# Kernel tuning notes

Measured on AMD Instinct MI355X. Metric: run time of the kernel, lower is better.

The kernel has to match this reference:

```python
import jax, jax.numpy as jnp
import numpy as np

BATCH, OUT, M, IN = 128, 256, 8, 512

def setup_inputs() -> dict:
    key = jax.random.key(0)
    k1, k2 = jax.random.split(key)
    x = jax.random.normal(k1, (BATCH, M, IN), dtype=jnp.float32)
    DNM_W = jax.random.normal(k2, (OUT, M, IN), dtype=jnp.float32)
    return {"x": x, "DNM_W": DNM_W}

def reference(x, DNM_W):
    # broadcast mul: (i,1,j,k) * (1,b,j,k) -> (i,b,j,k)
    z = jax.nn.sigmoid(x[:, None, :, :] * DNM_W[None, :, :, :])
    z = jnp.sum(z, axis=3)   # (i,b,j): sum over input_size
    z = jnp.prod(z, axis=2)  # (i,b):   prod over M branches
    # normalize(rate=1, dim=1): scale rows to sum 1, then standardize (unbiased std)
    total = jnp.sum(z, axis=1, keepdims=True)
    z = z / total
    mean = jnp.mean(z, axis=1, keepdims=True)
    std = jnp.std(z, axis=1, keepdims=True, ddof=1)  # torch.std is unbiased
    return (z - mean) / std
```

## Files before the change

kernel.cpp:

```cpp
#include <hip/hip_runtime.h>
#include <hip/hip_bf16.h>

#define BATCH 128
#define NOUT  256
#define MB    8
#define IN    512

#define THREADS 256
#define TI 32
#define TB 32
#define CH 128
#define CH4 (CH/4)
#define PLANE (BATCH*NOUT)

typedef float v2f __attribute__((ext_vector_type(2)));

__device__ __forceinline__ float fast_exp2(float v) {
#if __has_builtin(__builtin_amdgcn_exp2f)
  return __builtin_amdgcn_exp2f(v);
#else
  return exp2f(v);
#endif
}
__device__ __forceinline__ float fast_rcp(float v) {
#if __has_builtin(__builtin_amdgcn_rcpf)
  return __builtin_amdgcn_rcpf(v);
#else
  return 1.0f / v;
#endif
}

__device__ __forceinline__ float sig4(v2f p02, v2f p13) {
  float e0 = fast_exp2(p02.x), e2 = fast_exp2(p02.y);
  float e1 = fast_exp2(p13.x), e3 = fast_exp2(p13.y);
  v2f f02 = {e0, e2}; f02 += 1.0f;
  v2f f13 = {e1, e3}; f13 += 1.0f;
  v2f prod = f02 * f13;
  v2f sum  = f02 + f13;
  v2f prodsw = __builtin_shufflevector(prod, prod, 1, 0);
  v2f t = sum * prodsw;
  float num = t.x + t.y;
  float den = prod.x * prod.y;
  return num * fast_rcp(den);
}

template<int JPB, int KCB>
__global__ __launch_bounds__(THREADS, 4) void dnm_partial_kernel(
    const float* __restrict__ x, const float* __restrict__ w,
    float* __restrict__ part)
{
  __shared__ float4 xs4[TI * 32];
  __shared__ float4 ws4[TB * 32];

  const int t   = threadIdx.x;
  const int ti2 = t >> 4;
  const int tb2 = t & 15;
  const int b0  = blockIdx.x * TB;
  const int i0  = blockIdx.y * TI;
  constexpr int KG = (IN / CH) / KCB;
  const int j0  = (blockIdx.z / KG) * JPB;
  const int q0  = (blockIdx.z % KG) * KCB;

  const float4* gx = (const float4*)x;
  const float4* gw = (const float4*)w;
  const float NEG_LOG2E = -1.4426950408889634f;

  float p00 = 1.0f, p01 = 1.0f, p10 = 1.0f, p11 = 1.0f;
  #pragma unroll
  for (int jj = 0; jj < JPB; ++jj) {
    const int j = j0 + jj;
    float s00 = 0.0f, s01 = 0.0f, s10 = 0.0f, s11 = 0.0f;
    #pragma unroll
    for (int cc = 0; cc < KCB; ++cc) {
      const int q = q0 + cc;
      __syncthreads();
      #pragma unroll
      for (int p = 0; p < (2 * TI * CH4) / THREADS; ++p) {
        int idx = t + p * THREADS;
        int r = idx >> 5, c4 = idx & 31;
        int c4s = c4 ^ ((r >> 1) & 7);
        if (r < TI) {
          float4 xv = gx[(size_t)((i0 + r) * MB + j) * (IN / 4) + q * CH4 + c4];
          xv.x *= NEG_LOG2E; xv.y *= NEG_LOG2E; xv.z *= NEG_LOG2E; xv.w *= NEG_LOG2E;
          xs4[r * 32 + c4s] = xv;
        } else {
          ws4[(r - TI) * 32 + c4s] =
              gw[(size_t)((b0 + r - TI) * MB + j) * (IN / 4) + q * CH4 + c4];
        }
      }
      __syncthreads();
      const int sx = ti2 & 7, sw = tb2 & 7;
      const float4* __restrict__ xb0 = &xs4[(2 * ti2) * 32];
      const float4* __restrict__ wb0 = &ws4[(2 * tb2) * 32];
      #pragma unroll 4
      for (int k4 = 0; k4 < CH4; ++k4) {
        int kx = k4 ^ sx, kw = k4 ^ sw;
        float4 xv0 = xb0[kx], xv1 = xb0[32 + kx];
        float4 wv0 = wb0[kw], wv1 = wb0[32 + kw];
        v2f x0a = {xv0.x, xv0.z}, x0b = {xv0.y, xv0.w};
        v2f x1a = {xv1.x, xv1.z}, x1b = {xv1.y, xv1.w};
        v2f w0a = {wv0.x, wv0.z}, w0b = {wv0.y, wv0.w};
        v2f w1a = {wv1.x, wv1.z}, w1b = {wv1.y, wv1.w};
        s00 += sig4(x0a * w0a, x0b * w0b);
        s01 += sig4(x0a * w1a, x0b * w1b);
        s10 += sig4(x1a * w0a, x1b * w0b);
        s11 += sig4(x1a * w1a, x1b * w1b);
      }
    }
    p00 *= s00; p01 *= s01; p10 *= s10; p11 *= s11;
  }
  float* dst = part + (size_t)blockIdx.z * PLANE;
  const int i = i0 + 2 * ti2, b = b0 + 2 * tb2;
  dst[(size_t)i * NOUT + b]           = p00;
  dst[(size_t)i * NOUT + b + 1]       = p01;
  dst[(size_t)(i + 1) * NOUT + b]     = p10;
  dst[(size_t)(i + 1) * NOUT + b + 1] = p11;
}

__device__ __forceinline__ float block_sum(float v, float* red) {
  #pragma unroll
  for (int o = 32; o > 0; o >>= 1) v += __shfl_down(v, o, 64);
  int lane = threadIdx.x & 63, wid = threadIdx.x >> 6;
  __syncthreads();
  if (lane == 0) red[wid] = v;
  __syncthreads();
  return red[0] + red[1] + red[2] + red[3];
}

template<int JG, int KG>
__global__ __launch_bounds__(256) void dnm_norm_kernel(
    const float* __restrict__ part, float* __restrict__ out)
{
  __shared__ float red[4];
  const int i = blockIdx.x;
  const int t = threadIdx.x;
  float z = 1.0f;
  #pragma unroll
  for (int j = 0; j < JG; ++j) {
    float s = 0.0f;
    #pragma unroll
    for (int q = 0; q < KG; ++q)
      s += part[(size_t)(j * KG + q) * PLANE + (size_t)i * NOUT + t];
    z *= s;
  }
  float S  = block_sum(z, red);
  float zn = z / S;
  float m  = block_sum(zn, red) * (1.0f / NOUT);
  float dv = zn - m;
  float v  = block_sum(dv * dv, red) * (1.0f / (NOUT - 1));
  out[(size_t)i * NOUT + t] = dv / sqrtf(v);
}

extern "C" void kernel_launch(void* const* d_in, const int* in_sizes, int n_in,
                              void* d_out, int out_size, void* d_ws, size_t ws_size,
                              hipStream_t stream) {
  const float* x = (const float*)d_in[0];
  const float* w = (const float*)d_in[1];
  float* out = (float*)d_out;

  const size_t plane_bytes = (size_t)PLANE * sizeof(float);

  if (ws_size >= 32 * plane_bytes) {
    float* part = (float*)d_ws;
    dim3 gridA(NOUT / TB, BATCH / TI, 32);
    dnm_partial_kernel<1, 1><<<gridA, THREADS, 0, stream>>>(x, w, part);
    dnm_norm_kernel<8, 4><<<dim3(BATCH), 256, 0, stream>>>(part, out);
  } else if (ws_size >= plane_bytes) {
    float* part = (float*)d_ws;
    dim3 gridA(NOUT / TB, BATCH / TI, 1);
    dnm_partial_kernel<8, 4><<<gridA, THREADS, 0, stream>>>(x, w, part);
    dnm_norm_kernel<1, 1><<<dim3(BATCH), 256, 0, stream>>>(part, out);
  } else {
    float* part = out;
    dim3 gridA(NOUT / TB, BATCH / TI, 1);
    dnm_partial_kernel<8, 4><<<gridA, THREADS, 0, stream>>>(x, w, part);
    dnm_norm_kernel<1, 1><<<dim3(BATCH), 256, 0, stream>>>(part, out);
  }
}
```

Measured before the change: 86.70 us.

## Widen register tile to 2x4 outputs per thread with padded x shared layout

Each thread now computes a 2x4 block of (batch, out) sums instead of 2x2, with the out-tile doubled to 64 and the K chunk halved to 64, so the split-K grid grows to 64 planes. The x shared tile uses a padded stride of 17 float4 instead of an XOR swizzle, W keeps a swizzle keyed on groups of four rows, and partial results are written as float4. The aim is fewer shared-memory loads per sigmoid evaluation and wider stores. In exchange the norm kernel must read and sum twice as many partial planes, the workspace needed grows, and register pressure rises.

```diff
diff --git a/kernel.cpp b/kernel.cpp
--- a/kernel.cpp
+++ b/kernel.cpp
@@ -8,9 +8,10 @@
 
 #define THREADS 256
 #define TI 32
-#define TB 32
-#define CH 128
+#define TB 64
+#define CH 64
 #define CH4 (CH/4)
+#define XST 17
 #define PLANE (BATCH*NOUT)
 
 typedef float v2f __attribute__((ext_vector_type(2)));
@@ -39,9 +40,7 @@
   v2f sum  = f02 + f13;
   v2f prodsw = __builtin_shufflevector(prod, prod, 1, 0);
   v2f t = sum * prodsw;
-  float num = t.x + t.y;
-  float den = prod.x * prod.y;
-  return num * fast_rcp(den);
+  return (t.x + t.y) * fast_rcp(prod.x * prod.y);
 }
 
 template<int JPB, int KCB>
@@ -49,72 +48,82 @@
     const float* __restrict__ x, const float* __restrict__ w,
     float* __restrict__ part)
 {
-  __shared__ float4 xs4[TI * 32];
-  __shared__ float4 ws4[TB * 32];
+  __shared__ float4 xs4[TI * XST];
+  __shared__ float4 ws4[TB * CH4];
 
-  const int t   = threadIdx.x;
-  const int ti2 = t >> 4;
-  const int tb2 = t & 15;
-  const int b0  = blockIdx.x * TB;
-  const int i0  = blockIdx.y * TI;
+  const int t  = threadIdx.x;
+  const int ti = t >> 4;
+  const int n  = t & 15;
+  const int b0 = blockIdx.x * TB;
+  const int i0 = blockIdx.y * TI;
   constexpr int KG = (IN / CH) / KCB;
-  const int j0  = (blockIdx.z / KG) * JPB;
-  const int q0  = (blockIdx.z % KG) * KCB;
+  const int j0 = (blockIdx.z / KG) * JPB;
+  const int q0 = (blockIdx.z % KG) * KCB;
 
   const float4* gx = (const float4*)x;
   const float4* gw = (const float4*)w;
   const float NEG_LOG2E = -1.4426950408889634f;
 
-  float p00 = 1.0f, p01 = 1.0f, p10 = 1.0f, p11 = 1.0f;
+  float p00=1.f,p01=1.f,p02_=1.f,p03=1.f, p10=1.f,p11=1.f,p12=1.f,p13_=1.f;
   #pragma unroll
   for (int jj = 0; jj < JPB; ++jj) {
     const int j = j0 + jj;
-    float s00 = 0.0f, s01 = 0.0f, s10 = 0.0f, s11 = 0.0f;
+    float s00=0.f,s01=0.f,s02=0.f,s03=0.f, s10=0.f,s11=0.f,s12=0.f,s13=0.f;
     #pragma unroll
     for (int cc = 0; cc < KCB; ++cc) {
       const int q = q0 + cc;
       __syncthreads();
       #pragma unroll
-      for (int p = 0; p < (2 * TI * CH4) / THREADS; ++p) {
+      for (int p = 0; p < (TI + TB) * CH4 / THREADS; ++p) {
         int idx = t + p * THREADS;
-        int r = idx >> 5, c4 = idx & 31;
-        int c4s = c4 ^ ((r >> 1) & 7);
+        int r = idx >> 4, c4 = idx & 15;
         if (r < TI) {
           float4 xv = gx[(size_t)((i0 + r) * MB + j) * (IN / 4) + q * CH4 + c4];
           xv.x *= NEG_LOG2E; xv.y *= NEG_LOG2E; xv.z *= NEG_LOG2E; xv.w *= NEG_LOG2E;
-          xs4[r * 32 + c4s] = xv;
+          xs4[r * XST + c4] = xv;
         } else {
-          ws4[(r - TI) * 32 + c4s] =
-              gw[(size_t)((b0 + r - TI) * MB + j) * (IN / 4) + q * CH4 + c4];
+          int rw = r - TI;
+          int c4s = c4 ^ ((rw >> 2) & 7);
+          ws4[rw * CH4 + c4s] = gw[(size_t)((b0 + rw) * MB + j) * (IN / 4) + q * CH4 + c4];
         }
       }
       __syncthreads();
-      const int sx = ti2 & 7, sw = tb2 & 7;
-      const float4* __restrict__ xb0 = &xs4[(2 * ti2) * 32];
-      const float4* __restrict__ wb0 = &ws4[(2 * tb2) * 32];
+      const float4* __restrict__ xr0 = &xs4[(2 * ti)     * XST];
+      const float4* __restrict__ xr1 = &xs4[(2 * ti + 1) * XST];
+      const float4* __restrict__ wr  = &ws4[(4 * n) * CH4];
+      const int sw = n & 7;
       #pragma unroll 4
       for (int k4 = 0; k4 < CH4; ++k4) {
-        int kx = k4 ^ sx, kw = k4 ^ sw;
-        float4 xv0 = xb0[kx], xv1 = xb0[32 + kx];
-        float4 wv0 = wb0[kw], wv1 = wb0[32 + kw];
+        float4 xv0 = xr0[k4], xv1 = xr1[k4];
+        int kw = k4 ^ sw;
+        float4 wv0 = wr[0 * CH4 + kw];
+        float4 wv1 = wr[1 * CH4 + kw];
+        float4 wv2 = wr[2 * CH4 + kw];
+        float4 wv3 = wr[3 * CH4 + kw];
         v2f x0a = {xv0.x, xv0.z}, x0b = {xv0.y, xv0.w};
         v2f x1a = {xv1.x, xv1.z}, x1b = {xv1.y, xv1.w};
-        v2f w0a = {wv0.x, wv0.z}, w0b = {wv0.y, wv0.w};
-        v2f w1a = {wv1.x, wv1.z}, w1b = {wv1.y, wv1.w};
-        s00 += sig4(x0a * w0a, x0b * w0b);
-        s01 += sig4(x0a * w1a, x0b * w1b);
-        s10 += sig4(x1a * w0a, x1b * w0b);
-        s11 += sig4(x1a * w1a, x1b * w1b);
+        v2f wa, wb;
+        wa = (v2f){wv0.x, wv0.z}; wb = (v2f){wv0.y, wv0.w};
+        s00 += sig4(x0a * wa, x0b * wb);
+        s10 += sig4(x1a * wa, x1b * wb);
+        wa = (v2f){wv1.x, wv1.z}; wb = (v2f){wv1.y, wv1.w};
+        s01 += sig4(x0a * wa, x0b * wb);
+        s11 += sig4(x1a * wa, x1b * wb);
+        wa = (v2f){wv2.x, wv2.z}; wb = (v2f){wv2.y, wv2.w};
+        s02 += sig4(x0a * wa, x0b * wb);
+        s12 += sig4(x1a * wa, x1b * wb);
+        wa = (v2f){wv3.x, wv3.z}; wb = (v2f){wv3.y, wv3.w};
+        s03 += sig4(x0a * wa, x0b * wb);
+        s13 += sig4(x1a * wa, x1b * wb);
       }
     }
-    p00 *= s00; p01 *= s01; p10 *= s10; p11 *= s11;
+    p00 *= s00; p01 *= s01; p02_ *= s02; p03 *= s03;
+    p10 *= s10; p11 *= s11; p12 *= s12; p13_ *= s13;
   }
-  float* dst = part + (size_t)blockIdx.z * PLANE;
-  const int i = i0 + 2 * ti2, b = b0 + 2 * tb2;
-  dst[(size_t)i * NOUT + b]           = p00;
-  dst[(size_t)i * NOUT + b + 1]       = p01;
-  dst[(size_t)(i + 1) * NOUT + b]     = p10;
-  dst[(size_t)(i + 1) * NOUT + b + 1] = p11;
+  float4* dst = (float4*)(part + (size_t)blockIdx.z * PLANE);
+  const int i = i0 + 2 * ti, bq = (b0 >> 2) + n;
+  dst[(size_t)i * (NOUT / 4) + bq]       = make_float4(p00, p01, p02_, p03);
+  dst[(size_t)(i + 1) * (NOUT / 4) + bq] = make_float4(p10, p11, p12, p13_);
 }
 
 __device__ __forceinline__ float block_sum(float v, float* red) {
@@ -160,20 +169,20 @@
 
   const size_t plane_bytes = (size_t)PLANE * sizeof(float);
 
-  if (ws_size >= 32 * plane_bytes) {
+  if (ws_size >= 64 * plane_bytes) {
     float* part = (float*)d_ws;
-    dim3 gridA(NOUT / TB, BATCH / TI, 32);
+    dim3 gridA(NOUT / TB, BATCH / TI, 64);
     dnm_partial_kernel<1, 1><<<gridA, THREADS, 0, stream>>>(x, w, part);
-    dnm_norm_kernel<8, 4><<<dim3(BATCH), 256, 0, stream>>>(part, out);
+    dnm_norm_kernel<8, 8><<<dim3(BATCH), 256, 0, stream>>>(part, out);
   } else if (ws_size >= plane_bytes) {
     float* part = (float*)d_ws;
     dim3 gridA(NOUT / TB, BATCH / TI, 1);
-    dnm_partial_kernel<8, 4><<<gridA, THREADS, 0, stream>>>(x, w, part);
+    dnm_partial_kernel<8, 8><<<gridA, THREADS, 0, stream>>>(x, w, part);
     dnm_norm_kernel<1, 1><<<dim3(BATCH), 256, 0, stream>>>(part, out);
   } else {
     float* part = out;
     dim3 gridA(NOUT / TB, BATCH / TI, 1);
-    dnm_partial_kernel<8, 4><<<gridA, THREADS, 0, stream>>>(x, w, part);
+    dnm_partial_kernel<8, 8><<<gridA, THREADS, 0, stream>>>(x, w, part);
     dnm_norm_kernel<1, 1><<<dim3(BATCH), 256, 0, stream>>>(part, out);
   }
 }
```

Result: slower. 102.0 us (+17.7%).
